# Optimization experiments

Measured on AMD Instinct MI355X. Metric: run time of the kernel, lower is better.

The kernel has to match this reference:

```python
import jax, jax.numpy as jnp
import numpy as np

VOCAB = 128
OFFSET = 1.0
SCALE = 0.6
# token id -> expected duration for initials/voiced consonants
_IV_KEYS = np.array([94, 122, 100, 92, 43, 27])
_IV_VALS = np.array([2.0, 3.0, 2.0, 2.0, 5.0, 5.0], dtype=np.float32)
_RATIO_KEYS = np.array([44, 28, 29, 27, 121, 43])


def setup_inputs() -> dict:
    key = jax.random.key(0)
    k1, k2 = jax.random.split(key)
    B, T = 1024, 8192
    dur_pred = jax.random.uniform(k1, (B, T), dtype=jnp.float32)
    txt_tokens = jax.random.randint(k2, (B, T), 0, VOCAB, dtype=jnp.int64)
    return {"dur_pred": dur_pred, "txt_tokens": txt_tokens}


def _dur_rules(dur_pred, txt_tokens):
    # Vectorized equivalent of the sequential loop. Key observations:
    # 1) dur_rules[b, i] is always reset to dur_pred[b, i] at iteration i, so the
    #    rule-2 write to position i+1 is always overwritten (dead write).
    # 2) Each position i subtracts its own gaps (gap1 + gap2) and receives the
    #    gaps of position i+1 (propagation to i-1 only happens when i > 0).
    B, T = dur_pred.shape
    exp_tab = jnp.zeros((VOCAB,), dur_pred.dtype).at[_IV_KEYS].set(jnp.asarray(_IV_VALS, dur_pred.dtype))
    mask1_tab = jnp.zeros((VOCAB,), bool).at[_IV_KEYS].set(True)
    mask2_tab = jnp.zeros((VOCAB,), bool).at[_RATIO_KEYS].set(True)

    in1 = mask1_tab[txt_tokens]            # [B, T]
    expected = exp_tab[txt_tokens]          # [B, T]
    gap1 = jnp.where(in1 & (dur_pred > expected), dur_pred - expected, 0.0)

    nxt = jnp.pad(dur_pred[:, 1:], ((0, 0), (0, 1)))  # dur_pred[i+1], 0 at end
    has_next = (jnp.arange(T) < T - 1)[None, :]
    in2 = mask2_tab[txt_tokens]
    gap2 = jnp.where(in2 & has_next & (3.0 * dur_pred > nxt), dur_pred - nxt / 3.0, 0.0)

    g = gap1 + gap2
    g_next = jnp.pad(g[:, 1:], ((0, 0), (0, 1)))  # gap from position i+1
    return dur_pred - g + g_next


def reference(dur_pred, txt_tokens):
    dur_rules = _dur_rules(dur_pred, txt_tokens)
    a = jnp.log(dur_pred + OFFSET)
    b = jnp.log(dur_rules + OFFSET)
    return SCALE * jnp.mean((a - b) ** 2)
```

## Files before the change

### kernel.cpp

```cpp
#include <hip/hip_runtime.h>
#include <math.h>


constexpr int TT = 8192;
constexpr int BB = 1024;
constexpr int NBLK = 4096;
constexpr float LOSS_SCALE = 0.6f;

__global__ __launch_bounds__(256) void rules_partial(const float* __restrict__ dur,
                                                     const int* __restrict__ tok,
                                                     float* __restrict__ partial) {
    int blk = blockIdx.x;
    int row = blk >> 2, q = blk & 3;
    const float* dr = dur + (size_t)row * TT;
    const int*   tr = tok + (size_t)row * TT;
    int tid = (int)threadIdx.x;
    int i0 = q * 2048 + tid * 8;
    int lane = tid & 63;

    float4 da = *reinterpret_cast<const float4*>(dr + i0);
    float4 db = *reinterpret_cast<const float4*>(dr + i0 + 4);
    int4   ta = *reinterpret_cast<const int4*>(tr + i0);
    int4   tb = *reinterpret_cast<const int4*>(tr + i0 + 4);

    bool rowend = (q == 3) && (tid == 255);
    float hd8 = 0.0f, hd9 = 0.0f; int ht8 = 0;
    if (lane == 63 && !rowend) {
        float2 hh = *reinterpret_cast<const float2*>(dr + i0 + 8);
        hd8 = hh.x; hd9 = hh.y;
        ht8 = tr[i0 + 8];
    }

    __shared__ float lut[128];
    if (tid < 128) {
        int t = tid;
        float e1 = INFINITY;
        if (t == 94 || t == 100 || t == 92) e1 = 2.0f;
        else if (t == 122)                  e1 = 3.0f;
        else if (t == 43 || t == 27)        e1 = 5.0f;
        bool m2 = (t == 44 || t == 28 || t == 29 || t == 27 || t == 121 || t == 43);
        lut[t] = m2 ? -e1 : e1;
    }
    __syncthreads();

    float d[9];
    d[0]=da.x; d[1]=da.y; d[2]=da.z; d[3]=da.w;
    d[4]=db.x; d[5]=db.y; d[6]=db.z; d[7]=db.w;
    int tk[8] = {ta.x, ta.y, ta.z, ta.w, tb.x, tb.y, tb.z, tb.w};

    float d8s = __shfl_down(d[0], 1, 64);
    d[8] = (lane == 63) ? (rowend ? INFINITY : hd8) : d8s;

    float v[8];
#pragma unroll
    for (int j = 0; j < 8; ++j) v[j] = lut[tk[j] & 127];

    float g[9];
#pragma unroll
    for (int j = 0; j < 8; ++j) {
        float gap1 = fmaxf(d[j] - fabsf(v[j]), 0.0f);
        float gap2 = (v[j] < 0.0f)
                   ? fmaxf(fmaf(d[j+1], -(1.0f/3.0f), d[j]), 0.0f) : 0.0f;
        g[j] = gap1 + gap2;
    }

    float g8s = __shfl_down(g[0], 1, 64);
    if (lane == 63) {
        float hv = lut[ht8 & 127];
        float gap1 = fmaxf(hd8 - fabsf(hv), 0.0f);
        float gap2 = (hv < 0.0f)
                   ? fmaxf(fmaf(hd9, -(1.0f/3.0f), hd8), 0.0f) : 0.0f;
        g8s = rowend ? 0.0f : (gap1 + gap2);
    }
    g[8] = g8s;

    float acc = 0.0f;
#pragma unroll
    for (int j = 0; j < 8; ++j) {
        float dp1 = d[j] + 1.0f;
        float num = d[j] - g[j] + g[j + 1] + 1.0f;
        float c = __logf(__fdividef(num, dp1));
        acc = fmaf(c, c, acc);
    }

#pragma unroll
    for (int off = 32; off; off >>= 1) acc += __shfl_down(acc, off, 64);
    __shared__ float sred[4];
    int wid = tid >> 6;
    if (lane == 0) sred[wid] = acc;
    __syncthreads();
    if (tid == 0) partial[blk] = sred[0] + sred[1] + sred[2] + sred[3];
}

__global__ __launch_bounds__(1024) void rules_final(const float* __restrict__ partial,
                                                    float* __restrict__ out) {
    float acc = 0.0f;
    for (int i = (int)threadIdx.x; i < NBLK; i += 1024) acc += partial[i];
#pragma unroll
    for (int off = 32; off; off >>= 1) acc += __shfl_down(acc, off, 64);
    __shared__ float sred[16];
    int lane = threadIdx.x & 63, wid = threadIdx.x >> 6;
    if (lane == 0) sred[wid] = acc;
    __syncthreads();
    if (threadIdx.x == 0) {
        float total = 0.0f;
#pragma unroll
        for (int w = 0; w < 16; ++w) total += sred[w];
        out[0] = LOSS_SCALE * (total / (float)((long long)BB * TT));
    }
}

extern "C" void kernel_launch(void* const* d_in, const int* in_sizes, int n_in,
                              void* d_out, int out_size, void* d_ws, size_t ws_size,
                              hipStream_t stream) {
    const float* dur = (const float*)d_in[0];
    const int*   tok = (const int*)d_in[1];
    float* partial = (float*)d_ws;
    float* out = (float*)d_out;

    rules_partial<<<NBLK, 256, 0, stream>>>(dur, tok, partial);
    rules_final<<<1, 1024, 0, stream>>>(partial, out);
}
```

Measured before the change: 20.39 us.

## Process four chunks per block with software-pipelined loads

Cuts the grid from 4096 to 1024 blocks. Each block now handles four 2048-element chunks strided by 1024 blocks, and the next chunk's loads are issued before the current chunk's compute so memory latency overlaps with arithmetic. The LUT setup and final reduction are amortized over more work, and the final kernel reads one partial per thread. In exchange, register pressure rises from holding two chunks in flight, and there is less block-level parallelism to hide latency.

Result: slower. 23.24 us (+14.0%).

```diff
diff --git a/kernel.cpp b/kernel.cpp
--- a/kernel.cpp
+++ b/kernel.cpp
@@ -4,34 +4,79 @@
 
 constexpr int TT = 8192;
 constexpr int BB = 1024;
-constexpr int NBLK = 4096;
+constexpr int NBLK = 1024;
 constexpr float LOSS_SCALE = 0.6f;
+
+#define DECL_CHUNK(i) float4 DA##i, DB##i; int4 TA##i, TB##i; \
+    float hda##i, hdb##i; int hta##i; bool re##i;
+
+#define LOAD_CHUNK(i, cidx) { \
+    int c_ = (cidx); int row_ = c_ >> 2, q_ = c_ & 3; \
+    const float* dr_ = dur + (size_t)row_ * TT; \
+    const int*   tr_ = tok + (size_t)row_ * TT; \
+    int i0_ = q_ * 2048 + tid * 8; \
+    DA##i = *reinterpret_cast<const float4*>(dr_ + i0_); \
+    DB##i = *reinterpret_cast<const float4*>(dr_ + i0_ + 4); \
+    TA##i = *reinterpret_cast<const int4*>(tr_ + i0_); \
+    TB##i = *reinterpret_cast<const int4*>(tr_ + i0_ + 4); \
+    re##i = (q_ == 3) && (tid == 255); \
+    hda##i = 0.0f; hdb##i = 0.0f; hta##i = 0; \
+    if (lane == 63 && !re##i) { \
+        float2 hh_ = *reinterpret_cast<const float2*>(dr_ + i0_ + 8); \
+        hda##i = hh_.x; hdb##i = hh_.y; \
+        hta##i = tr_[i0_ + 8]; \
+    } \
+}
+
+#define COMPUTE_CHUNK(i) { \
+    float d[9]; \
+    d[0]=DA##i.x; d[1]=DA##i.y; d[2]=DA##i.z; d[3]=DA##i.w; \
+    d[4]=DB##i.x; d[5]=DB##i.y; d[6]=DB##i.z; d[7]=DB##i.w; \
+    int tk[8] = {TA##i.x, TA##i.y, TA##i.z, TA##i.w, \
+                 TB##i.x, TB##i.y, TB##i.z, TB##i.w}; \
+    float d8s_ = __shfl_down(d[0], 1, 64); \
+    d[8] = (lane == 63) ? (re##i ? INFINITY : hda##i) : d8s_; \
+    float g[9]; \
+    _Pragma("unroll") \
+    for (int j = 0; j < 8; ++j) { \
+        float v_ = lut[tk[j] & 127]; \
+        float gap1_ = fmaxf(d[j] - fabsf(v_), 0.0f); \
+        float gap2_ = (v_ < 0.0f) \
+                    ? fmaxf(fmaf(d[j+1], -(1.0f/3.0f), d[j]), 0.0f) : 0.0f; \
+        g[j] = gap1_ + gap2_; \
+    } \
+    float g8s_ = __shfl_down(g[0], 1, 64); \
+    if (lane == 63) { \
+        float hv_ = lut[hta##i & 127]; \
+        float gap1_ = fmaxf(hda##i - fabsf(hv_), 0.0f); \
+        float gap2_ = (hv_ < 0.0f) \
+                    ? fmaxf(fmaf(hdb##i, -(1.0f/3.0f), hda##i), 0.0f) : 0.0f; \
+        g8s_ = re##i ? 0.0f : (gap1_ + gap2_); \
+    } \
+    g[8] = g8s_; \
+    _Pragma("unroll") \
+    for (int j = 0; j < 8; ++j) { \
+        float dp1_ = d[j] + 1.0f; \
+        float num_ = d[j] - g[j] + g[j + 1] + 1.0f; \
+        float c_ = __logf(__fdividef(num_, dp1_)); \
+        acc = fmaf(c_, c_, acc); \
+    } \
+}
 
 __global__ __launch_bounds__(256) void rules_partial(const float* __restrict__ dur,
                                                      const int* __restrict__ tok,
                                                      float* __restrict__ partial) {
-    int blk = blockIdx.x;
-    int row = blk >> 2, q = blk & 3;
-    const float* dr = dur + (size_t)row * TT;
-    const int*   tr = tok + (size_t)row * TT;
     int tid = (int)threadIdx.x;
-    int i0 = q * 2048 + tid * 8;
     int lane = tid & 63;
-
-    float4 da = *reinterpret_cast<const float4*>(dr + i0);
-    float4 db = *reinterpret_cast<const float4*>(dr + i0 + 4);
-    int4   ta = *reinterpret_cast<const int4*>(tr + i0);
-    int4   tb = *reinterpret_cast<const int4*>(tr + i0 + 4);
-
-    bool rowend = (q == 3) && (tid == 255);
-    float hd8 = 0.0f, hd9 = 0.0f; int ht8 = 0;
-    if (lane == 63 && !rowend) {
-        float2 hh = *reinterpret_cast<const float2*>(dr + i0 + 8);
-        hd8 = hh.x; hd9 = hh.y;
-        ht8 = tr[i0 + 8];
-    }
+    int bid = (int)blockIdx.x;
 
     __shared__ float lut[128];
+
+    DECL_CHUNK(0) DECL_CHUNK(1) DECL_CHUNK(2) DECL_CHUNK(3)
+
+    LOAD_CHUNK(0, bid)
+    LOAD_CHUNK(1, bid + 1024)
+
     if (tid < 128) {
         int t = tid;
         float e1 = INFINITY;
@@ -43,45 +88,13 @@
     }
     __syncthreads();
 
-    float d[9];
-    d[0]=da.x; d[1]=da.y; d[2]=da.z; d[3]=da.w;
-    d[4]=db.x; d[5]=db.y; d[6]=db.z; d[7]=db.w;
-    int tk[8] = {ta.x, ta.y, ta.z, ta.w, tb.x, tb.y, tb.z, tb.w};
-
-    float d8s = __shfl_down(d[0], 1, 64);
-    d[8] = (lane == 63) ? (rowend ? INFINITY : hd8) : d8s;
-
-    float v[8];
-#pragma unroll
-    for (int j = 0; j < 8; ++j) v[j] = lut[tk[j] & 127];
-
-    float g[9];
-#pragma unroll
-    for (int j = 0; j < 8; ++j) {
-        float gap1 = fmaxf(d[j] - fabsf(v[j]), 0.0f);
-        float gap2 = (v[j] < 0.0f)
-                   ? fmaxf(fmaf(d[j+1], -(1.0f/3.0f), d[j]), 0.0f) : 0.0f;
-        g[j] = gap1 + gap2;
-    }
-
-    float g8s = __shfl_down(g[0], 1, 64);
-    if (lane == 63) {
-        float hv = lut[ht8 & 127];
-        float gap1 = fmaxf(hd8 - fabsf(hv), 0.0f);
-        float gap2 = (hv < 0.0f)
-                   ? fmaxf(fmaf(hd9, -(1.0f/3.0f), hd8), 0.0f) : 0.0f;
-        g8s = rowend ? 0.0f : (gap1 + gap2);
-    }
-    g[8] = g8s;
-
     float acc = 0.0f;
-#pragma unroll
-    for (int j = 0; j < 8; ++j) {
-        float dp1 = d[j] + 1.0f;
-        float num = d[j] - g[j] + g[j + 1] + 1.0f;
-        float c = __logf(__fdividef(num, dp1));
-        acc = fmaf(c, c, acc);
-    }
+    COMPUTE_CHUNK(0)
+    LOAD_CHUNK(2, bid + 2048)
+    COMPUTE_CHUNK(1)
+    LOAD_CHUNK(3, bid + 3072)
+    COMPUTE_CHUNK(2)
+    COMPUTE_CHUNK(3)
 
 #pragma unroll
     for (int off = 32; off; off >>= 1) acc += __shfl_down(acc, off, 64);
@@ -89,13 +102,12 @@
     int wid = tid >> 6;
     if (lane == 0) sred[wid] = acc;
     __syncthreads();
-    if (tid == 0) partial[blk] = sred[0] + sred[1] + sred[2] + sred[3];
+    if (tid == 0) partial[bid] = sred[0] + sred[1] + sred[2] + sred[3];
 }
 
 __global__ __launch_bounds__(1024) void rules_final(const float* __restrict__ partial,
                                                     float* __restrict__ out) {
-    float acc = 0.0f;
-    for (int i = (int)threadIdx.x; i < NBLK; i += 1024) acc += partial[i];
+    float acc = partial[threadIdx.x];
 #pragma unroll
     for (int off = 32; off; off >>= 1) acc += __shfl_down(acc, off, 64);
     __shared__ float sred[16];
```
